# Optimization experiments

Hardware: AMD Instinct MI355X
Metric: run time of the kernel (lower is better)

## Reference

```python
import jax, jax.numpy as jnp
import numpy as np

B, T, D, H = 4, 3072, 1024, 16
HD = D // H

def setup_inputs() -> dict:
    key = jax.random.key(0)
    ks = jax.random.split(key, 7)
    s = 1.0 / np.sqrt(D)
    x = jax.random.normal(ks[0], (B, T, D), dtype=jnp.float32)
    Wq = jax.random.normal(ks[1], (D, D), dtype=jnp.float32) * s
    Wk = jax.random.normal(ks[2], (D, D), dtype=jnp.float32) * s
    Wv = jax.random.normal(ks[3], (D, D), dtype=jnp.float32) * s
    Wo = jax.random.normal(ks[4], (D, D), dtype=jnp.float32) * s
    bo = jnp.zeros((D,), dtype=jnp.float32)
    Wconv = jax.random.normal(ks[5], (D, D, 3), dtype=jnp.float32) * (1.0 / np.sqrt(3 * D))  # (out, in, kw)
    return {"x": x, "Wq": Wq, "Wk": Wk, "Wv": Wv, "Wo": Wo, "bo": bo, "Wconv": Wconv}

def reference(x, Wq, Wk, Wv, Wo, bo, Wconv):
    b, t, d = x.shape
    # stride-3 conv pooling of K/V stream (Conv1d(D, D, 3, stride=3, bias=False))
    kc = jax.lax.conv_general_dilated(
        x.transpose(0, 2, 1), Wconv, window_strides=(3,), padding='VALID',
        dimension_numbers=('NCH', 'OIH', 'NCH')).transpose(0, 2, 1)  # (B, T//3, D)
    k_tmp = jnp.concatenate([x[:, :1, :], kc], axis=1)  # (B, Tk, D)
    tk = k_tmp.shape[1]
    # comparison-based bias mask: masked where 3*k_idx >= q_idx + 0.001
    q_idx = jnp.arange(t, dtype=jnp.float32)
    k_idx = jnp.arange(tk, dtype=jnp.float32)
    mask = (k_idx[None, :] * 3.0 >= q_idx[:, None] + 0.001).astype(x.dtype)  # (T, Tk)
    # projections (torch Linear: y = x @ W.T)
    q = x @ Wq.T
    k = k_tmp @ Wk.T
    v = k_tmp @ Wv.T
    q = q.reshape(b, t, H, HD).transpose(0, 2, 1, 3)   # (B, H, T, HD)
    k = k.reshape(b, tk, H, HD).transpose(0, 2, 1, 3)  # (B, H, Tk, HD)
    v = v.reshape(b, tk, H, HD).transpose(0, 2, 1, 3)
    scores = jnp.einsum('bhqd,bhkd->bhqk', q, k) * (HD ** -0.5)
    scores = scores + mask * jnp.asarray(-1e9, dtype=x.dtype)
    p = jax.nn.softmax(scores, axis=-1)  # dropout is identity in eval (p=0)
    o = jnp.einsum('bhqk,bhkd->bhqd', p, v)
    o = o.transpose(0, 2, 1, 3).reshape(b, t, d)
    return o @ Wo.T + bo
```

## Files before the change

### kernel.cpp

```cpp
#include <hip/hip_runtime.h>
#include <hip/hip_bf16.h>
#include <cstdint>
#include <cstddef>

typedef __attribute__((ext_vector_type(8))) __bf16 bf16x8;
typedef __attribute__((ext_vector_type(4))) __bf16 bf16x4;
typedef __attribute__((ext_vector_type(4))) float  floatx4;

#define MFMA16x16x32(a, b, c) __builtin_amdgcn_mfma_f32_16x16x32_bf16((a), (b), (c), 0, 0, 0)

#define ATTN_SC 0.18033688011112042f

__device__ __forceinline__ void gload_lds16(const void* g, void* l) {
  __builtin_amdgcn_global_load_lds((const __attribute__((address_space(1))) void*)g,
                                   (__attribute__((address_space(3))) void*)l,
                                   16, 0, 0);
}


__global__ void prep_kernel(const float* __restrict__ x,
                            const float* __restrict__ Wq, const float* __restrict__ Wk,
                            const float* __restrict__ Wv, const float* __restrict__ Wo,
                            const float* __restrict__ Wconv,
                            __bf16* __restrict__ xb,
                            __bf16* __restrict__ wqb, __bf16* __restrict__ wkb,
                            __bf16* __restrict__ wvb, __bf16* __restrict__ wob,
                            __bf16* __restrict__ wc2, __bf16* __restrict__ ktmp) {
  const int bid = blockIdx.x, tid = threadIdx.x;
  if (bid < 4096) {
    const int which = bid >> 10;
    const float* src = (which == 0) ? Wq : (which == 1) ? Wk : (which == 2) ? Wv : Wo;
    __bf16* dst = (which == 0) ? wqb : (which == 1) ? wkb : (which == 2) ? wvb : wob;
    const int i = (bid & 1023) * 256 + tid;
    floatx4 v = *(const floatx4*)(src + (size_t)i * 4);
    bf16x4 o; o[0] = (__bf16)v[0]; o[1] = (__bf16)v[1]; o[2] = (__bf16)v[2]; o[3] = (__bf16)v[3];
    *(bf16x4*)(dst + (size_t)i * 4) = o;
  } else if (bid < 5120) {
    const int t = (bid - 4096) * 256 + tid;
    const int o = t >> 8, c = t & 255;
    const float* base = Wconv + (size_t)o * 3072 + c * 12;
    float f[12];
    *(floatx4*)(f)     = *(const floatx4*)(base);
    *(floatx4*)(f + 4) = *(const floatx4*)(base + 4);
    *(floatx4*)(f + 8) = *(const floatx4*)(base + 8);
#pragma unroll
    for (int kw = 0; kw < 3; ++kw) {
      bf16x4 q;
#pragma unroll
      for (int j = 0; j < 4; ++j) q[j] = (__bf16)f[3 * j + kw];
      *(bf16x4*)(wc2 + (size_t)o * 3072 + kw * 1024 + c * 4) = q;
    }
  } else if (bid < 5136) {
    const int i = (bid - 5120) * 256 + tid;
    const int b = i >> 10, c = i & 1023;
    ktmp[(size_t)b * 1025 * 1024 + c] = (__bf16)x[(size_t)b * 3072 * 1024 + c];
  } else {
    const int i = (bid - 5136) * 256 + tid;
    floatx4 v = *(const floatx4*)(x + (size_t)i * 4);
    bf16x4 o; o[0] = (__bf16)v[0]; o[1] = (__bf16)v[1]; o[2] = (__bf16)v[2]; o[3] = (__bf16)v[3];
    *(bf16x4*)(xb + (size_t)i * 4) = o;
  }
}

__global__ void vtrans_kernel(const __bf16* __restrict__ V, __bf16* __restrict__ Vt) {
  __shared__ __attribute__((aligned(16))) __bf16 tile[64][72];
  const int tid = threadIdx.x;
  const int bh = blockIdx.y;
  const int b = bh >> 4, h = bh & 15;
  const int t0 = blockIdx.x * 64;
  const int r = tid >> 3, s = tid & 7;
#pragma unroll
  for (int p = 0; p < 2; ++p) {
    const int t = p * 32 + r;
    bf16x8 v = *(const bf16x8*)(V + ((size_t)(b * 1025 + t0 + t)) * 1024 + h * 64 + s * 8);
    *(bf16x8*)(&tile[t][s * 8]) = v;
  }
  __syncthreads();
#pragma unroll
  for (int p = 0; p < 2; ++p) {
    const int d = p * 32 + r;
    bf16x8 o;
#pragma unroll
    for (int e = 0; e < 8; ++e) o[e] = tile[s * 8 + e][d];
    *(bf16x8*)(Vt + ((size_t)bh * 64 + d) * 1024 + t0 + s * 8) = o;
  }
}


template <int MODE>
__device__ __forceinline__ void gemm8_body(
    const __bf16* __restrict__ A, const __bf16* __restrict__ Bw, void* __restrict__ Cout,
    const float* __restrict__ bias, int N, int K, int m0, int n0,
    __bf16* As, __bf16* Bs)
{
  const int tid  = threadIdx.x;
  const int wave = tid >> 6;
  const int lane = tid & 63;
  const int g    = lane >> 4;
  const int ln   = lane & 15;
  const int wr   = (wave >> 2) * 64;
  const int wc   = (wave & 3) * 64;

  const int prow = tid >> 3;
  const int pc   = tid & 7;
  const int ca   = pc ^ (prow & 7);
  const size_t aSrc  = (size_t)(m0 + prow + ((ca >> 2) << 6)) * K + ((ca & 3) << 3);
  const size_t bSrc0 = (size_t)(n0 + prow + ((ca >> 2) << 7)) * K + ((ca & 3) << 3);
  const size_t bSrc1 = bSrc0 + (size_t)64 * K;

  int aOff[4], bOff[4];
#pragma unroll
  for (int i = 0; i < 4; ++i) {
    const int ra = wr + i * 16 + ln;
    const int pr = ra & 63;
    const int c  = ((ra >> 6) << 2) + g;
    aOff[i] = pr * 64 + ((c ^ (pr & 7)) << 3);
  }
#pragma unroll
  for (int j = 0; j < 4; ++j) {
    const int rb = wc + j * 16 + ln;
    const int pr = rb & 127;
    const int c  = ((rb >> 7) << 2) + g;
    bOff[j] = pr * 64 + ((c ^ (pr & 7)) << 3);
  }

  floatx4 acc[4][4];
#pragma unroll
  for (int i = 0; i < 4; ++i)
#pragma unroll
    for (int j = 0; j < 4; ++j) { floatx4 z = {0.f, 0.f, 0.f, 0.f}; acc[i][j] = z; }

  __bf16* const ad0 = As + (tid << 3);
  __bf16* const bd0 = Bs + (tid << 3);

  auto STAGE = [&](int t, int half) {
    const int koff = t * 64 + ((half & 1) << 5);
    gload_lds16(A  + aSrc  + koff, ad0 + (half << 12));
    gload_lds16(Bw + bSrc0 + koff, bd0 + (half << 13));
    gload_lds16(Bw + bSrc1 + koff, bd0 + (half << 13) + 4096);
  };

  auto COMPUTE = [&](int half) {
    __builtin_amdgcn_sched_barrier(0);
    const __bf16* ah = As + (half << 12);
    const __bf16* bh = Bs + (half << 13);
    bf16x8 af[4], bf[4];
#pragma unroll
    for (int i = 0; i < 4; ++i) af[i] = *(const bf16x8*)(ah + aOff[i]);
#pragma unroll
    for (int j = 0; j < 4; ++j) bf[j] = *(const bf16x8*)(bh + bOff[j]);
    asm volatile("s_waitcnt lgkmcnt(0)" ::: "memory");
    __builtin_amdgcn_sched_barrier(0);
    __builtin_amdgcn_s_setprio(1);
#pragma unroll
    for (int i = 0; i < 4; ++i)
#pragma unroll
      for (int j = 0; j < 4; ++j)
        acc[i][j] = MFMA16x16x32(af[i], bf[j], acc[i][j]);
    __builtin_amdgcn_s_setprio(0);
  };

  STAGE(0, 0);
  STAGE(0, 1);
  const int HT = K >> 5;
  for (int h = 0; h < HT - 2; ++h) {
    STAGE((h + 2) >> 1, (h + 2) & 3);
    asm volatile("s_waitcnt vmcnt(6)" ::: "memory");
    __builtin_amdgcn_s_barrier();
    COMPUTE(h & 3);
    __builtin_amdgcn_s_barrier();
  }
  asm volatile("s_waitcnt vmcnt(3)" ::: "memory");
  __builtin_amdgcn_s_barrier();
  COMPUTE((HT - 2) & 3);
  asm volatile("s_waitcnt vmcnt(0)" ::: "memory");
  __builtin_amdgcn_s_barrier();
  COMPUTE((HT - 1) & 3);

#pragma unroll
  for (int j = 0; j < 4; ++j) {
    const int col = n0 + wc + j * 16 + ln;
    float bj = 0.f;
    if (MODE == 2) bj = bias[col];
#pragma unroll
    for (int i = 0; i < 4; ++i)
#pragma unroll
      for (int r = 0; r < 4; ++r) {
        const int row = m0 + wr + i * 16 + g * 4 + r;
        if (MODE == 2) {
          ((float*)Cout)[(size_t)row * N + col] = acc[i][j][r] + bj;
        } else if (MODE == 1) {
          const size_t orow = (size_t)(row >> 10) * 1025 + 1 + (row & 1023);
          ((__bf16*)Cout)[orow * 1024 + col] = (__bf16)acc[i][j][r];
        } else if (MODE == 4) {
          ((__bf16*)Cout)[(size_t)row * N + col] = (__bf16)(acc[i][j][r] * ATTN_SC);
        } else {
          ((__bf16*)Cout)[(size_t)row * N + col] = (__bf16)acc[i][j][r];
        }
      }
  }
}

__global__ __launch_bounds__(512, 2) void gemm_convq_kernel(
    const __bf16* __restrict__ xb, const __bf16* __restrict__ wc2,
    const __bf16* __restrict__ wqb, __bf16* __restrict__ ktmp, __bf16* __restrict__ qb)
{
  __shared__ __attribute__((aligned(16))) __bf16 As[16384];
  __shared__ __attribute__((aligned(16))) __bf16 Bs[32768];
  const int xcd = blockIdx.x & 7, s = blockIdx.x >> 3;
  if (s < 16) {
    const int id = xcd * 16 + s;
    gemm8_body<1>(xb, wc2, ktmp, nullptr, 1024, 3072, (id >> 2) * 128, (id & 3) * 256, As, Bs);
  } else {
    const int id = xcd * 48 + (s - 16);
    gemm8_body<4>(xb, wqb, qb, nullptr, 1024, 1024, (id >> 2) * 128, (id & 3) * 256, As, Bs);
  }
}

__global__ __launch_bounds__(512, 2) void gemm_kv_kernel(
    const __bf16* __restrict__ ktmp, const __bf16* __restrict__ wkb,
    const __bf16* __restrict__ wvb, __bf16* __restrict__ kb, __bf16* __restrict__ vb)
{
  __shared__ __attribute__((aligned(16))) __bf16 As[16384];
  __shared__ __attribute__((aligned(16))) __bf16 Bs[32768];
  const int id = (blockIdx.x & 7) * 33 + (blockIdx.x >> 3);
  const int p  = (id >= 132) ? 1 : 0;
  const int rest = id - p * 132;
  gemm8_body<0>(ktmp, p ? wvb : wkb, p ? vb : kb, nullptr, 1024, 1024,
                (rest >> 2) * 128, (rest & 3) * 256, As, Bs);
}

__global__ __launch_bounds__(512, 2) void gemm_o_kernel(
    const __bf16* __restrict__ ob, const __bf16* __restrict__ wob,
    float* __restrict__ out, const float* __restrict__ bo)
{
  __shared__ __attribute__((aligned(16))) __bf16 As[16384];
  __shared__ __attribute__((aligned(16))) __bf16 Bs[32768];
  const int id = (blockIdx.x & 7) * 48 + (blockIdx.x >> 3);
  gemm8_body<2>(ob, wob, out, bo, 1024, 1024, (id >> 2) * 128, (id & 3) * 256, As, Bs);
}


__global__ __launch_bounds__(256) void attn_kernel(
    const __bf16* __restrict__ Q, const __bf16* __restrict__ Kk,
    const __bf16* __restrict__ Vt, __bf16* __restrict__ O)
{
  __shared__ __attribute__((aligned(16))) __bf16 Kd[2][64 * 64];
  __shared__ __attribute__((aligned(16))) __bf16 Vd[2][64 * 64];
  __shared__ __attribute__((aligned(16))) __bf16 Ps[4][32 * 64];

  const int tid  = threadIdx.x;
  const int wave = tid >> 6;
  const int lane = tid & 63;
  const int g    = lane >> 4;
  const int ln   = lane & 15;

  const int l    = blockIdx.x;
  const int xcd  = l & 7;
  const int b    = xcd >> 1;
  const int rest = l >> 3;
  const int h    = rest & 15;
  const int qt   = ((11 - (rest >> 4)) << 1) | (xcd & 1);
  const int q0   = qt * 128 + wave * 32;

  const size_t qrow0 = (size_t)b * 3072 + q0;
  const size_t krow0 = (size_t)b * 1025;
  const size_t vtrow = ((size_t)(b * 16 + h)) * 64;
  const int hc = h * 64;
  const int sw = (ln & 7) << 3;
  __bf16* Pw = Ps[wave];

  const int srow = lane >> 3;
  const int scol = (lane & 7) * 8;

  auto stage = [&](int kt, int bb) {
    const int kb0 = kt * 64;
#pragma unroll
    for (int i = 0; i < 2; ++i) {
      const int rr = (wave * 2 + i) * 8 + srow;
      gload_lds16(Kk + (krow0 + kb0 + rr) * 1024 + hc + scol,
                  Kd[bb] + (size_t)rr * 64 + scol);
      gload_lds16(Vt + (vtrow + rr) * 1024 + kb0 + scol,
                  Vd[bb] + (size_t)rr * 64 + scol);
    }
  };

  bf16x8 qf[2][2];
#pragma unroll
  for (int i = 0; i < 2; ++i)
#pragma unroll
    for (int kc = 0; kc < 2; ++kc)
      qf[i][kc] = *(const bf16x8*)(Q + (qrow0 + i * 16 + ln) * 1024 + hc + kc * 32 + g * 8);

  floatx4 oacc[2][4];
  floatx4 oal[2];
#pragma unroll
  for (int i = 0; i < 2; ++i) {
    floatx4 z = {0.f, 0.f, 0.f, 0.f};
    oal[i] = z;
#pragma unroll
    for (int dt = 0; dt < 4; ++dt) oacc[i][dt] = z;
  }

  bf16x8 ones;
#pragma unroll
  for (int e = 0; e < 8; ++e) ones[e] = (__bf16)1.0f;

  const int nkt_blk = (((qt * 128 + 127) / 3) >> 6) + 1;
  const int nfull   = (q0 >= 189) ? ((q0 - 189) / 192 + 1) : 0;

  stage(0, 0);

  for (int kt = 0; kt < nkt_blk; ++kt) {
    const int bb = kt & 1;
    __syncthreads();
    if (kt + 1 < nkt_blk) stage(kt + 1, bb ^ 1);
    const int kb0 = kt * 64;
    const bool masked = (kt >= nfull);

    bf16x8 kf[4][2];
#pragma unroll
    for (int jk = 0; jk < 4; ++jk)
#pragma unroll
      for (int kc = 0; kc < 2; ++kc)
        kf[jk][kc] = *(const bf16x8*)(Kd[bb] + (jk * 16 + ln) * 64 + kc * 32 + g * 8);

#pragma unroll
    for (int jk = 0; jk < 4; ++jk)
#pragma unroll
      for (int i = 0; i < 2; ++i) {
        floatx4 s = {0.f, 0.f, 0.f, 0.f};
        s = MFMA16x16x32(kf[jk][0], qf[i][0], s);
        s = MFMA16x16x32(kf[jk][1], qf[i][1], s);
        float p[4];
#pragma unroll
        for (int r = 0; r < 4; ++r) {
          float e = __builtin_amdgcn_exp2f(s[r]);
          if (masked) {
            const int key = kb0 + jk * 16 + 4 * g + r;
            const int q   = q0 + i * 16 + ln;
            e = (3 * key <= q) ? e : 0.f;
          }
          p[r] = e;
        }
        bf16x4 pk;
        pk[0] = (__bf16)p[0]; pk[1] = (__bf16)p[1]; pk[2] = (__bf16)p[2]; pk[3] = (__bf16)p[3];
        *(bf16x4*)(Pw + (i * 16 + ln) * 64 + ((jk * 16 + 4 * g) ^ sw)) = pk;
      }

#pragma unroll
    for (int kc = 0; kc < 2; ++kc) {
      bf16x8 pf0 = *(const bf16x8*)(Pw + (ln) * 64      + ((kc * 32 + g * 8) ^ sw));
      bf16x8 pf1 = *(const bf16x8*)(Pw + (16 + ln) * 64 + ((kc * 32 + g * 8) ^ sw));
      oal[0] = MFMA16x16x32(ones, pf0, oal[0]);
      oal[1] = MFMA16x16x32(ones, pf1, oal[1]);
#pragma unroll
      for (int dt = 0; dt < 4; ++dt) {
        bf16x8 vf = *(const bf16x8*)(Vd[bb] + (dt * 16 + ln) * 64 + kc * 32 + g * 8);
        oacc[0][dt] = MFMA16x16x32(vf, pf0, oacc[0][dt]);
        oacc[1][dt] = MFMA16x16x32(vf, pf1, oacc[1][dt]);
      }
    }
  }

#pragma unroll
  for (int i = 0; i < 2; ++i) {
    const float inv = 1.0f / oal[i][0];
    const size_t row = qrow0 + i * 16 + ln;
#pragma unroll
    for (int dt = 0; dt < 4; ++dt) {
      bf16x4 o4;
#pragma unroll
      for (int r = 0; r < 4; ++r) o4[r] = (__bf16)(oacc[i][dt][r] * inv);
      *(bf16x4*)(O + row * 1024 + hc + dt * 16 + 4 * g) = o4;
    }
  }
}


extern "C" void kernel_launch(void* const* d_in, const int* in_sizes, int n_in,
                              void* d_out, int out_size, void* d_ws, size_t ws_size,
                              hipStream_t stream) {
  (void)in_sizes; (void)n_in; (void)out_size; (void)ws_size;
  const float* x     = (const float*)d_in[0];
  const float* Wq    = (const float*)d_in[1];
  const float* Wk    = (const float*)d_in[2];
  const float* Wv    = (const float*)d_in[3];
  const float* Wo    = (const float*)d_in[4];
  const float* bo    = (const float*)d_in[5];
  const float* Wconv = (const float*)d_in[6];

  char* ws = (char*)d_ws;
  const size_t SZ_XQ = (size_t)12288 * 1024 * 2;
  const size_t SZ_KT = (size_t)4224 * 1024 * 2;
  const size_t SZ_W  = (size_t)1024 * 1024 * 2;

  __bf16* xb   = (__bf16*)(ws);
  __bf16* qb   = (__bf16*)(ws + SZ_XQ);
  __bf16* ktmp = (__bf16*)(ws + 2 * SZ_XQ);
  __bf16* kb   = (__bf16*)(ws + 2 * SZ_XQ + SZ_KT);
  __bf16* vb   = (__bf16*)(ws + 2 * SZ_XQ + 2 * SZ_KT);
  __bf16* wqb  = (__bf16*)(ws + 2 * SZ_XQ + 3 * SZ_KT);
  __bf16* wkb  = (__bf16*)(ws + 2 * SZ_XQ + 3 * SZ_KT + SZ_W);
  __bf16* wvb  = (__bf16*)(ws + 2 * SZ_XQ + 3 * SZ_KT + 2 * SZ_W);
  __bf16* wob  = (__bf16*)(ws + 2 * SZ_XQ + 3 * SZ_KT + 3 * SZ_W);
  __bf16* wc2  = (__bf16*)(ws + 2 * SZ_XQ + 3 * SZ_KT + 4 * SZ_W);
  __bf16* vt   = xb;

  prep_kernel<<<dim3(17424), dim3(256), 0, stream>>>(x, Wq, Wk, Wv, Wo, Wconv,
                                                     xb, wqb, wkb, wvb, wob, wc2, ktmp);
  gemm_convq_kernel<<<dim3(512), dim3(512), 0, stream>>>(xb, wc2, wqb, ktmp, qb);
  gemm_kv_kernel<<<dim3(264), dim3(512), 0, stream>>>(ktmp, wkb, wvb, kb, vb);
  vtrans_kernel<<<dim3(16, 64), dim3(256), 0, stream>>>(vb, vt);
  attn_kernel<<<dim3(1536), dim3(256), 0, stream>>>(qb, kb, vt, qb);
  gemm_o_kernel<<<dim3(384), dim3(512), 0, stream>>>(qb, wob, (float*)d_out, bo);
}
```

Measured before the change: 377.7 us.

## Deepen GEMM LDS prefetch to three stages and overlap fragment reads

Restructures the GEMM main loop to keep three half-tiles in flight in a four-slot LDS ring instead of two. Each iteration reads its LDS fragments first, then issues the next global-to-LDS load and waits for the following slot before running the MFMAs. The aim is to hide more global-memory latency and overlap LDS reads with outstanding loads. The cost is a larger in-flight window and more intricate vmcnt bookkeeping, where a miscount would read stale LDS data.

```diff
diff --git a/kernel.cpp b/kernel.cpp
--- a/kernel.cpp
+++ b/kernel.cpp
@@ -133,24 +133,41 @@
   __bf16* const ad0 = As + (tid << 3);
   __bf16* const bd0 = Bs + (tid << 3);
 
-  auto STAGE = [&](int t, int half) {
-    const int koff = t * 64 + ((half & 1) << 5);
-    gload_lds16(A  + aSrc  + koff, ad0 + (half << 12));
-    gload_lds16(Bw + bSrc0 + koff, bd0 + (half << 13));
-    gload_lds16(Bw + bSrc1 + koff, bd0 + (half << 13) + 4096);
+  auto STAGE = [&](int halfidx) {
+    const int slot = halfidx & 3;
+    const int koff = (halfidx >> 1) * 64 + ((halfidx & 1) << 5);
+    gload_lds16(A  + aSrc  + koff, ad0 + (slot << 12));
+    gload_lds16(Bw + bSrc0 + koff, bd0 + (slot << 13));
+    gload_lds16(Bw + bSrc1 + koff, bd0 + (slot << 13) + 4096);
   };
 
-  auto COMPUTE = [&](int half) {
-    __builtin_amdgcn_sched_barrier(0);
-    const __bf16* ah = As + (half << 12);
-    const __bf16* bh = Bs + (half << 13);
+  const int HT = K >> 5;
+
+  STAGE(0); STAGE(1); STAGE(2);
+  asm volatile("s_waitcnt vmcnt(6)" ::: "memory");
+  __builtin_amdgcn_s_barrier();
+  __builtin_amdgcn_sched_barrier(0);
+
+  for (int h = 0; h < HT; ++h) {
+    const int slot = h & 3;
+    const __bf16* ah = As + (slot << 12);
+    const __bf16* bh = Bs + (slot << 13);
     bf16x8 af[4], bf[4];
 #pragma unroll
     for (int i = 0; i < 4; ++i) af[i] = *(const bf16x8*)(ah + aOff[i]);
 #pragma unroll
     for (int j = 0; j < 4; ++j) bf[j] = *(const bf16x8*)(bh + bOff[j]);
-    asm volatile("s_waitcnt lgkmcnt(0)" ::: "memory");
-    __builtin_amdgcn_sched_barrier(0);
+
+    if (h + 3 < HT) STAGE(h + 3);
+
+    if (h + 1 < HT) {
+      if (h + 3 < HT)      { asm volatile("s_waitcnt vmcnt(6)" ::: "memory"); }
+      else if (h + 2 < HT) { asm volatile("s_waitcnt vmcnt(3)" ::: "memory"); }
+      else                 { asm volatile("s_waitcnt vmcnt(0)" ::: "memory"); }
+      __builtin_amdgcn_s_barrier();
+      __builtin_amdgcn_sched_barrier(0);
+    }
+
     __builtin_amdgcn_s_setprio(1);
 #pragma unroll
     for (int i = 0; i < 4; ++i)
@@ -158,24 +175,12 @@
       for (int j = 0; j < 4; ++j)
         acc[i][j] = MFMA16x16x32(af[i], bf[j], acc[i][j]);
     __builtin_amdgcn_s_setprio(0);
-  };
-
-  STAGE(0, 0);
-  STAGE(0, 1);
-  const int HT = K >> 5;
-  for (int h = 0; h < HT - 2; ++h) {
-    STAGE((h + 2) >> 1, (h + 2) & 3);
-    asm volatile("s_waitcnt vmcnt(6)" ::: "memory");
-    __builtin_amdgcn_s_barrier();
-    COMPUTE(h & 3);
-    __builtin_amdgcn_s_barrier();
-  }
-  asm volatile("s_waitcnt vmcnt(3)" ::: "memory");
-  __builtin_amdgcn_s_barrier();
-  COMPUTE((HT - 2) & 3);
-  asm volatile("s_waitcnt vmcnt(0)" ::: "memory");
-  __builtin_amdgcn_s_barrier();
-  COMPUTE((HT - 1) & 3);
+
+    if (h + 1 < HT) {
+      __builtin_amdgcn_s_barrier();
+      __builtin_amdgcn_sched_barrier(0);
+    }
+  }
 
 #pragma unroll
   for (int j = 0; j < 4; ++j) {
```

New measurement: 341.4 us. -9.6%, faster.
